# Kernel tuning notes

Measured on AMD Instinct MI355X. Metric: run time of the kernel, lower is better.

Reference implementation:

```python
import jax, jax.numpy as jnp
import numpy as np
from jax import lax

# norse LIFParameters defaults: dt=1e-3, tau_mem_inv=100, tau_syn_inv=200, v_leak=0, v_reset=0
ALPHA = 100.0
DT_TM = 0.1   # dt * tau_mem_inv
DT_TS = 0.2   # dt * tau_syn_inv

@jax.custom_vjp
def superspike(x):
    # Heaviside forward, SuperSpike surrogate gradient backward
    return (x > 0).astype(x.dtype)

def _ss_fwd(x):
    return superspike(x), x

def _ss_bwd(x, g):
    return (g / (ALPHA * jnp.abs(x) + 1.0) ** 2,)

superspike.defvjp(_ss_fwd, _ss_bwd)

def lif_step(inp, v, i, v_th):
    # norse lif_feed_forward_step (feedforward LIF cell)
    v_dec = v + DT_TM * (i - v)           # v_leak = 0
    i_dec = i * (1.0 - DT_TS)
    z = superspike(v_dec - v_th)
    v_new = (1.0 - z) * v_dec             # reset to v_reset = 0 on spike
    return z, v_new, i_dec + inp

def conv2d(x, w):
    return lax.conv_general_dilated(x, w, (1, 1), 'VALID',
                                    dimension_numbers=('NCHW', 'OIHW', 'NCHW'))

def avg_pool2(x):
    s = lax.reduce_window(x, jnp.zeros((), x.dtype), lax.add,
                          (1, 1, 2, 2), (1, 1, 2, 2), 'VALID')
    return s * jnp.asarray(0.25, x.dtype)

def setup_inputs() -> dict:
    key = jax.random.key(0)
    ks = jax.random.split(key, 6)
    x = jax.random.uniform(ks[0], (40, 256, 1, 28, 28), dtype=jnp.float32)
    # kaiming-ish scales (1/sqrt(fan_in))
    w_conv1 = jax.random.normal(ks[1], (20, 1, 3, 3), jnp.float32) * (1.0 / np.sqrt(9))
    w_conv2 = jax.random.normal(ks[2], (50, 20, 3, 3), jnp.float32) * (1.0 / np.sqrt(180))
    w_fc1 = jax.random.normal(ks[3], (500, 6050), jnp.float32) * (1.0 / np.sqrt(6050))
    w_fc2 = jax.random.normal(ks[4], (200, 500), jnp.float32) * (1.0 / np.sqrt(500))
    w_fc_out = jax.random.normal(ks[5], (10, 200), jnp.float32) * (1.0 / np.sqrt(200))
    return {"x": x, "w_conv1": w_conv1, "w_conv2": w_conv2,
            "w_fc1": w_fc1, "w_fc2": w_fc2, "w_fc_out": w_fc_out}

def reference(x, w_conv1, w_conv2, w_fc1, w_fc2, w_fc_out):
    T, B = x.shape[0], x.shape[1]
    dt = x.dtype
    z0 = jnp.zeros((B, 20, 26, 26), dt)
    z1 = jnp.zeros((B, 50, 11, 11), dt)
    z2 = jnp.zeros((B, 500), dt)
    z3 = jnp.zeros((B, 200), dt)
    zo = jnp.zeros((B, 10), dt)
    carry0 = (z0, z0, z1, z1, z2, z2, z3, z3, zo, zo)

    def step(carry, xt):
        v0, i0, v1, i1, v2, i2, v3, i3, vo, io = carry
        z = conv2d(xt, w_conv1)
        z, v0, i0 = lif_step(z, v0, i0, 0.2)
        z = avg_pool2(z)
        z = conv2d(z, w_conv2)
        z, v1, i1 = lif_step(z, v1, i1, 0.2)
        z = z.reshape(B, -1)                      # [B, 50*11*11]
        z = z @ w_fc1.T
        z, v2, i2 = lif_step(z, v2, i2, 0.1)
        z = z @ w_fc2.T
        z, v3, i3 = lif_step(z, v3, i3, 0.05)
        z = z @ w_fc_out.T
        # LICell (norse li_feed_forward_step): output is decayed membrane voltage
        v_dec = vo + DT_TM * (io - vo)
        i_new = io * (1.0 - DT_TS) + z
        return (v0, i0, v1, i1, v2, i2, v3, i3, v_dec, i_new), v_dec

    _, voltages = lax.scan(step, carry0, x)
    return voltages  # [T, B, output_neurons]
```

## Files before the change

kernel.cpp:

```cpp
#include <hip/hip_runtime.h>
#include <hip/hip_bf16.h>

typedef _Float16 f16x8 __attribute__((ext_vector_type(8)));
typedef float f32x4  __attribute__((ext_vector_type(4)));
typedef unsigned short u16x4 __attribute__((ext_vector_type(4)));

#define T_STEPS 40
#define BATCH   256
#define S2LO    0.000244140625f

__device__ __forceinline__ unsigned short f2h_bits(float f) {
    union { _Float16 h; unsigned short u; } c; c.h = (_Float16)f; return c.u;
}

__device__ __forceinline__ float lif_update(float inp, float& v, float& i, float vth) {
    float vd = __fadd_rn(v, __fmul_rn(0.1f, __fsub_rn(i, v)));
    float id = __fmul_rn(0.8f, i);
    float z  = (vd > vth) ? 1.0f : 0.0f;
    v = (vd > vth) ? 0.0f : vd;
    i = __fadd_rn(id, inp);
    return z;
}

__device__ __forceinline__ void llds16(const unsigned short* g, void* l) {
    __builtin_amdgcn_global_load_lds(
        (const __attribute__((address_space(1))) unsigned int*)g,
        (__attribute__((address_space(3))) unsigned int*)l, 16, 0, 0);
}

__global__ __launch_bounds__(512) void k_conv1(
    const float* __restrict__ x,
    const float* __restrict__ w1,
    unsigned char* __restrict__ s0)
{
    const int b    = blockIdx.y;
    const int tid  = threadIdx.x;
    const int cell = blockIdx.x*512 + tid;
    const bool active = cell < 3380;
    const int pos  = cell / 20;
    const int oc   = cell % 20;
    const int pr   = pos / 13, q = pos % 13;
    const int r0   = 2*pr, c0 = 2*q;

    __shared__ __align__(16) float xl[2][784];

    float wr[9];
    if (active) {
        #pragma unroll
        for (int j = 0; j < 9; ++j) wr[j] = w1[oc*9 + j];
    }
    float vs[2][2], is[2][2];
    #pragma unroll
    for (int dr = 0; dr < 2; ++dr)
        #pragma unroll
        for (int dc = 0; dc < 2; ++dc) { vs[dr][dc] = 0.f; is[dr][dc] = 0.f; }

    if (tid < 196) {
        const float4* xs4 = (const float4*)(x + (size_t)b*784);
        *(float4*)&xl[0][tid*4] = xs4[tid];
    }

    for (int t = 0; t < T_STEPS; ++t) {
        __syncthreads();
        if (t + 1 < T_STEPS && tid < 196) {
            const float4* xs4 = (const float4*)(x + (size_t)((t+1)*BATCH + b)*784);
            *(float4*)&xl[(t+1)&1][tid*4] = xs4[tid];
        }
        const float* xc = xl[t&1];
        size_t base = (size_t)(t*BATCH + b) * 4096;

        if (active) {
            float tle[4][4];
            #pragma unroll
            for (int r = 0; r < 4; ++r)
                #pragma unroll
                for (int c = 0; c < 4; ++c)
                    tle[r][c] = xc[(r0 + r)*28 + c0 + c];
            int zsum = 0;
            #pragma unroll
            for (int dr = 0; dr < 2; ++dr)
                #pragma unroll
                for (int dc = 0; dc < 2; ++dc) {
                    float acc = 0.f;
                    #pragma unroll
                    for (int kr = 0; kr < 3; ++kr)
                        #pragma unroll
                        for (int kc = 0; kc < 3; ++kc)
                            acc += tle[dr+kr][dc+kc] * wr[kr*3+kc];
                    float z = lif_update(acc, vs[dr][dc], is[dr][dc], 0.2f);
                    zsum += (z > 0.5f) ? 1 : 0;
                }
            s0[base + (size_t)pos*24 + oc] = (unsigned char)zsum;
        } else {
            int p2 = cell - 3380;
            for (int idx = p2; idx < 716; idx += 204) {
                if (idx < 676) s0[base + (size_t)(idx >> 2)*24 + 20 + (idx & 3)] = 0;
                else           s0[base + 4056 + (idx - 676)] = 0;
            }
        }
    }
}

__global__ __launch_bounds__(256, 2) void k_conv2(
    const unsigned char* __restrict__ s0,
    const float* __restrict__ w2,
    unsigned short* __restrict__ z1)
{
    const int b    = blockIdx.x >> 1;
    const int half = blockIdx.x & 1;
    const int tid  = threadIdx.x;
    const int wv   = tid >> 6;
    const int lane = tid & 63;
    const int l15  = lane & 15;
    const int kg   = lane >> 4;
    const int wm   = wv;

    __shared__ __align__(16) unsigned short w2h[32*232];
    __shared__ __align__(16) unsigned short w2m[32*232];
    __shared__ __align__(16) unsigned short sIn[2*4096];

    for (int s = tid; s < 32*232; s += 256) {
        int ocw = s / 232, kk = s % 232;
        int g = kk / 24, ic = kk % 24;
        int oc = half*32 + ocw;
        float val = 0.f;
        if (oc < 50 && g < 9 && ic < 20) val = w2[(oc*20 + ic)*9 + g];
        _Float16 h = (_Float16)val;
        float r1 = (val - (float)h) * 4096.0f;
        union { _Float16 h; unsigned short u; } ch, cm;
        ch.h = h; cm.h = (_Float16)r1;
        w2h[s] = ch.u;
        w2m[s] = cm.u;
    }

    f16x8 bfrH[2][7];
    int addrA[2][7];
    #pragma unroll
    for (int mt = 0; mt < 2; ++mt) {
        int pos = wm*32 + mt*16 + l15;
        #pragma unroll
        for (int kt = 0; kt < 7; ++kt) {
            int k = kt*32 + kg*8;
            int g = k / 24, o = k - g*24;
            if (pos <= 120 && g <= 8) {
                int in_idx = pos + 2*(pos/11) + 13*(g/3) + (g % 3);
                addrA[mt][kt] = in_idx*48 + o*2;
            } else addrA[mt][kt] = 8128;
        }
    }

    {
        const unsigned char* srow = s0 + (size_t)(0*BATCH + b)*4096;
        uint4 raw = *(const uint4*)(srow + tid*16);
        unsigned short hv[16];
        #pragma unroll
        for (int w = 0; w < 4; ++w) {
            unsigned int u = ((const unsigned int*)&raw)[w];
            #pragma unroll
            for (int j = 0; j < 4; ++j)
                hv[w*4+j] = f2h_bits(0.25f * (float)((u >> (8*j)) & 0xFFu));
        }
        unsigned short* dst = sIn + tid*16;
        *(f16x8*)dst       = *(const f16x8*)&hv[0];
        *(f16x8*)(dst + 8) = *(const f16x8*)&hv[8];
    }
    __syncthreads();

    #pragma unroll
    for (int nt = 0; nt < 2; ++nt) {
        int n = nt*16 + l15;
        #pragma unroll
        for (int kt = 0; kt < 7; ++kt)
            bfrH[nt][kt] = *(const f16x8*)&w2h[n*232 + kt*32 + kg*8];
    }

    float vst[2][2][4], ist[2][2][4];
    #pragma unroll
    for (int mt = 0; mt < 2; ++mt)
        #pragma unroll
        for (int nt = 0; nt < 2; ++nt)
            #pragma unroll
            for (int r = 0; r < 4; ++r) { vst[mt][nt][r] = 0.f; ist[mt][nt][r] = 0.f; }

    const f32x4 zero4 = {0.f, 0.f, 0.f, 0.f};

    for (int t = 0; t < T_STEPS; ++t) {
        if (t > 0) __syncthreads();

        uint4 raw;
        if (t + 1 < T_STEPS)
            raw = *(const uint4*)(s0 + (size_t)((t+1)*BATCH + b)*4096 + tid*16);

        const char* curB = (const char*)(sIn + (t&1)*4096);

        f32x4 acch[2][2], accl[2][2];
        #pragma unroll
        for (int mt = 0; mt < 2; ++mt)
            #pragma unroll
            for (int nt = 0; nt < 2; ++nt) { acch[mt][nt] = zero4; accl[mt][nt] = zero4; }

        #pragma unroll
        for (int kt = 0; kt < 7; ++kt) {
            f16x8 bm[2];
            #pragma unroll
            for (int nt = 0; nt < 2; ++nt) {
                int n = nt*16 + l15, k = kt*32 + kg*8;
                bm[nt] = *(const f16x8*)&w2m[n*232 + k];
            }
            #pragma unroll
            for (int mt = 0; mt < 2; ++mt) {
                f16x8 a = *(const f16x8*)(curB + addrA[mt][kt]);
                #pragma unroll
                for (int nt = 0; nt < 2; ++nt) {
                    acch[mt][nt] = __builtin_amdgcn_mfma_f32_16x16x32_f16(
                        a, bfrH[nt][kt], acch[mt][nt], 0, 0, 0);
                    accl[mt][nt] = __builtin_amdgcn_mfma_f32_16x16x32_f16(
                        a, bm[nt], accl[mt][nt], 0, 0, 0);
                }
            }
        }

        size_t rowoff = (size_t)(t*BATCH + b) * 6208;
        #pragma unroll
        for (int mt = 0; mt < 2; ++mt) {
            int posb = wm*32 + mt*16 + kg*4;
            #pragma unroll
            for (int nt = 0; nt < 2; ++nt) {
                int ocn = half*32 + nt*16 + l15;
                u16x4 pack;
                #pragma unroll
                for (int r = 0; r < 4; ++r) {
                    float inp = __fadd_rn(acch[mt][nt][r], __fmul_rn(S2LO, accl[mt][nt][r]));
                    float z = lif_update(inp, vst[mt][nt][r], ist[mt][nt][r], 0.2f);
                    int pos = posb + r;
                    pack[r] = (pos <= 120 && z > 0.5f) ? (unsigned short)0x3C00 : (unsigned short)0;
                }
                if (ocn < 50 && posb < 121)
                    *(u16x4*)(z1 + rowoff + ocn*124 + posb) = pack;
            }
        }
        if (half == 0 && tid < 8) z1[rowoff + 6200 + tid] = 0;

        if (t + 1 < T_STEPS) {
            unsigned short hv[16];
            #pragma unroll
            for (int w = 0; w < 4; ++w) {
                unsigned int u = ((const unsigned int*)&raw)[w];
                #pragma unroll
                for (int j = 0; j < 4; ++j)
                    hv[w*4+j] = f2h_bits(0.25f * (float)((u >> (8*j)) & 0xFFu));
            }
            unsigned short* dst = sIn + ((t+1)&1)*4096 + tid*16;
            *(f16x8*)dst       = *(const f16x8*)&hv[0];
            *(f16x8*)(dst + 8) = *(const f16x8*)&hv[8];
        }
    }
}

__global__ __launch_bounds__(256, 4) void k_gemm_fc1(
    const unsigned short* __restrict__ A,
    const unsigned short* __restrict__ Bhi,
    const unsigned short* __restrict__ Blo,
    float* __restrict__ P)
{
    __shared__ __align__(16) unsigned short As[128*64];
    __shared__ __align__(16) unsigned short Bh[64*64];
    __shared__ __align__(16) unsigned short Bl[64*64];

    const int tid  = threadIdx.x;
    const int lane = tid & 63;
    const int wv   = tid >> 6;
    const int wm   = wv & 1, wn = wv >> 1;
    const int l15  = lane & 15, kg = lane >> 4;

    const int bid   = blockIdx.x;
    const int chunk = (bid & 7) * 160 + (bid >> 3);
    const int mb    = chunk >> 4;
    const int nn    = chunk & 15;
    const int mbase = mb * 128;
    const int nbase = (nn >> 1) * 64;
    const int kz    = nn & 1;
    const int kb0   = kz * 3136;
    const int kiters = 49 - kz;

    float* Pz = P + (size_t)kz * 5242880;

    const f32x4 zero4 = {0.f, 0.f, 0.f, 0.f};
    f32x4 acch[4][2], accl[4][2];
    #pragma unroll
    for (int mt = 0; mt < 4; ++mt)
        #pragma unroll
        for (int nt = 0; nt < 2; ++nt) { acch[mt][nt] = zero4; accl[mt][nt] = zero4; }

    const int rowA = tid >> 3;
    const int sw   = (((tid & 7) ^ (rowA & 7))) * 8;
    char* ldsA = (char*)As + (size_t)wv*1024;
    char* ldsH = (char*)Bh + (size_t)wv*1024;
    char* ldsL = (char*)Bl + (size_t)wv*1024;

    for (int ki = 0; ki < kiters; ++ki) {
        int kb = kb0 + ki * 64;
        #pragma unroll
        for (int c = 0; c < 4; ++c)
            llds16(A + (size_t)(mbase + c*32 + rowA)*6208 + kb + sw, ldsA + c*4096);
        #pragma unroll
        for (int c = 0; c < 2; ++c) {
            llds16(Bhi + (size_t)(nbase + c*32 + rowA)*6208 + kb + sw, ldsH + c*4096);
            llds16(Blo + (size_t)(nbase + c*32 + rowA)*6208 + kb + sw, ldsL + c*4096);
        }
        __syncthreads();
        #pragma unroll
        for (int kt = 0; kt < 2; ++kt) {
            f16x8 bh[2], bl[2], afv[4];
            #pragma unroll
            for (int nt = 0; nt < 2; ++nt) {
                int rb = wn*32 + nt*16 + l15;
                int ch = ((kt*4 + kg) ^ (rb & 7)) * 8;
                bh[nt] = *(const f16x8*)&Bh[rb*64 + ch];
                bl[nt] = *(const f16x8*)&Bl[rb*64 + ch];
            }
            #pragma unroll
            for (int mt = 0; mt < 4; ++mt) {
                int ra = wm*64 + mt*16 + l15;
                int ch = ((kt*4 + kg) ^ (ra & 7)) * 8;
                afv[mt] = *(const f16x8*)&As[ra*64 + ch];
            }
            #pragma unroll
            for (int mt = 0; mt < 4; ++mt)
                #pragma unroll
                for (int nt = 0; nt < 2; ++nt) {
                    acch[mt][nt] = __builtin_amdgcn_mfma_f32_16x16x32_f16(
                        afv[mt], bh[nt], acch[mt][nt], 0, 0, 0);
                    accl[mt][nt] = __builtin_amdgcn_mfma_f32_16x16x32_f16(
                        afv[mt], bl[nt], accl[mt][nt], 0, 0, 0);
                }
        }
        __syncthreads();
    }

    #pragma unroll
    for (int mt = 0; mt < 4; ++mt) {
        int m0 = mbase + wm*64 + mt*16 + kg*4;
        #pragma unroll
        for (int nt = 0; nt < 2; ++nt) {
            int n = nbase + wn*32 + nt*16 + l15;
            #pragma unroll
            for (int r = 0; r < 4; ++r) {
                float s = __fadd_rn(acch[mt][nt][r], __fmul_rn(S2LO, accl[mt][nt][r]));
                Pz[(size_t)(m0 + r)*512 + n] = s;
            }
        }
    }
}

__global__ __launch_bounds__(256, 3) void k_gemm(
    const unsigned short* __restrict__ A,
    const unsigned short* __restrict__ B0,
    float* __restrict__ C0,
    int Kp, int kiters, int ldc, int nstore,
    size_t strideB, size_t strideC)
{
    __shared__ __align__(16) unsigned short As[128*64];
    __shared__ __align__(16) unsigned short Bs[128*64];
    const unsigned short* B = B0 + (size_t)blockIdx.z * strideB;
    float* C = C0 + (size_t)blockIdx.z * strideC;

    const int tid  = threadIdx.x;
    const int lane = tid & 63;
    const int wv   = tid >> 6;
    const int wm   = wv & 1, wn = wv >> 1;
    const int l15  = lane & 15, kg = lane >> 4;
    const int mbase = blockIdx.x * 128;
    const int nbase = blockIdx.y * 128;

    const f32x4 zero4 = {0.f, 0.f, 0.f, 0.f};
    f32x4 acc[4][4];
    #pragma unroll
    for (int mt = 0; mt < 4; ++mt)
        #pragma unroll
        for (int nt = 0; nt < 4; ++nt) acc[mt][nt] = zero4;

    const int rowA = tid >> 3;
    const int sw   = (((tid & 7) ^ (rowA & 7))) * 8;
    char* ldsA = (char*)As + (size_t)wv*1024;
    char* ldsB = (char*)Bs + (size_t)wv*1024;

    for (int ki = 0; ki < kiters; ++ki) {
        int kb = ki * 64;
        #pragma unroll
        for (int c = 0; c < 4; ++c) {
            int row = c*32 + rowA;
            llds16(A + (size_t)(mbase + row)*Kp + kb + sw, ldsA + c*4096);
            llds16(B + (size_t)(nbase + row)*Kp + kb + sw, ldsB + c*4096);
        }
        __syncthreads();
        #pragma unroll
        for (int kt = 0; kt < 2; ++kt) {
            f16x8 bfv[4], afv[4];
            #pragma unroll
            for (int nt = 0; nt < 4; ++nt) {
                int rb = wn*64 + nt*16 + l15;
                int ch = ((kt*4 + kg) ^ (rb & 7)) * 8;
                bfv[nt] = *(const f16x8*)&Bs[rb*64 + ch];
            }
            #pragma unroll
            for (int mt = 0; mt < 4; ++mt) {
                int ra = wm*64 + mt*16 + l15;
                int ch = ((kt*4 + kg) ^ (ra & 7)) * 8;
                afv[mt] = *(const f16x8*)&As[ra*64 + ch];
            }
            #pragma unroll
            for (int mt = 0; mt < 4; ++mt)
                #pragma unroll
                for (int nt = 0; nt < 4; ++nt)
                    acc[mt][nt] = __builtin_amdgcn_mfma_f32_16x16x32_f16(
                        afv[mt], bfv[nt], acc[mt][nt], 0, 0, 0);
        }
        __syncthreads();
    }

    #pragma unroll
    for (int mt = 0; mt < 4; ++mt) {
        int m0 = mbase + wm*64 + mt*16 + kg*4;
        #pragma unroll
        for (int nt = 0; nt < 4; ++nt) {
            int n = nbase + wn*64 + nt*16 + l15;
            if (n < nstore) {
                #pragma unroll
                for (int r = 0; r < 4; ++r)
                    C[(size_t)(m0 + r)*ldc + n] = acc[mt][nt][r];
            }
        }
    }
}

__global__ void k_pack_all(
    const float* __restrict__ wf1, const float* __restrict__ wf2,
    const float* __restrict__ wfo,
    unsigned short* __restrict__ W1, unsigned short* __restrict__ W2,
    unsigned short* __restrict__ Wo)
{
    int idx = blockIdx.x*256 + threadIdx.x;
    float v; unsigned short *hi, *lo; int off;
    if (idx < 3178496) {
        int n = idx / 6208, k = idx - n*6208;
        int oc = k / 124, pos = k - oc*124;
        v = (n < 500 && oc < 50 && pos < 121) ? wf1[n*6050 + oc*121 + pos] : 0.f;
        hi = W1; lo = W1 + 3178496; off = idx;
    } else if (idx < 3178496 + 131072) {
        int i2 = idx - 3178496;
        int n = i2 >> 9, k = i2 & 511;
        v = (n < 200 && k < 500) ? wf2[n*500 + k] : 0.f;
        hi = W2; lo = W2 + 131072; off = i2;
    } else if (idx < 3178496 + 131072 + 32768) {
        int i3 = idx - 3178496 - 131072;
        int n = i3 >> 8, k = i3 & 255;
        v = (n < 10 && k < 200) ? wfo[n*200 + k] : 0.f;
        hi = Wo; lo = Wo + 32768; off = i3;
    } else return;
    _Float16 h = (_Float16)v;
    float r1 = (v - (float)h) * 4096.0f;
    union { _Float16 h; unsigned short u; } ch, cl;
    ch.h = h; cl.h = (_Float16)r1;
    hi[off] = ch.u;
    lo[off] = cl.u;
}

__global__ __launch_bounds__(512) void k_lif_scan(
    const float* __restrict__ c0, size_t pstride,
    unsigned short* __restrict__ zout,
    int ld, int nvalid, float vth, float pscale)
{
    int b = blockIdx.x;
    int n = threadIdx.x;
    float v = 0.f, cur = 0.f;
    const float* sx = c0 + (size_t)b*ld + n;
    const float* sy = sx + pstride;
    const size_t step = (size_t)BATCH*ld;
    float x0 = sx[0],      y0 = sy[0];
    float x1 = sx[step],   y1 = sy[step];
    float x2 = sx[2*step], y2 = sy[2*step];
    float x3 = sx[3*step], y3 = sy[3*step];

    #define LIF_SUB(J, XV, YV)                                                \
        {                                                                     \
            float s = __fadd_rn(XV, __fmul_rn(pscale, YV));                   \
            float z = lif_update(s, v, cur, vth);                             \
            zout[(size_t)((t+J)*BATCH + b)*ld + n] =                          \
                (n < nvalid && z > 0.5f) ? (unsigned short)0x3C00             \
                                         : (unsigned short)0;                 \
            if (t + J + 4 < T_STEPS) {                                        \
                XV = sx[(size_t)(t + J + 4)*step];                            \
                YV = sy[(size_t)(t + J + 4)*step];                            \
            }                                                                 \
        }

    for (int t = 0; t < T_STEPS; t += 4) {
        LIF_SUB(0, x0, y0);
        LIF_SUB(1, x1, y1);
        LIF_SUB(2, x2, y2);
        LIF_SUB(3, x3, y3);
    }
    #undef LIF_SUB
}

__global__ void k_li(const float* __restrict__ c0, size_t pstride,
                     float* __restrict__ out) {
    int g = blockIdx.x*64 + threadIdx.x;
    if (g >= 2560) return;
    int b = g / 10, n = g - b*10;
    const float* sx = c0 + (size_t)b*16 + n;
    const float* sy = sx + pstride;
    const size_t step = (size_t)BATCH*16;
    float vo = 0.f, io = 0.f;
    float x0 = sx[0],      y0 = sy[0];
    float x1 = sx[step],   y1 = sy[step];
    float x2 = sx[2*step], y2 = sy[2*step];
    float x3 = sx[3*step], y3 = sy[3*step];

    #define LI_SUB(J, XV, YV)                                                 \
        {                                                                     \
            float s = __fadd_rn(XV, __fmul_rn(S2LO, YV));                     \
            float vd = __fadd_rn(vo, __fmul_rn(0.1f, __fsub_rn(io, vo)));     \
            out[(size_t)((t+J)*BATCH + b)*10 + n] = vd;                       \
            io = __fadd_rn(__fmul_rn(0.8f, io), s);                           \
            vo = vd;                                                          \
            if (t + J + 4 < T_STEPS) {                                        \
                XV = sx[(size_t)(t + J + 4)*step];                            \
                YV = sy[(size_t)(t + J + 4)*step];                            \
            }                                                                 \
        }

    for (int t = 0; t < T_STEPS; t += 4) {
        LI_SUB(0, x0, y0);
        LI_SUB(1, x1, y1);
        LI_SUB(2, x2, y2);
        LI_SUB(3, x3, y3);
    }
    #undef LI_SUB
}

extern "C" void kernel_launch(void* const* d_in, const int* in_sizes, int n_in,
                              void* d_out, int out_size, void* d_ws, size_t ws_size,
                              hipStream_t stream) {
    (void)in_sizes; (void)n_in; (void)out_size; (void)ws_size;
    const float* x   = (const float*)d_in[0];
    const float* w1  = (const float*)d_in[1];
    const float* w2  = (const float*)d_in[2];
    const float* wf1 = (const float*)d_in[3];
    const float* wf2 = (const float*)d_in[4];
    const float* wfo = (const float*)d_in[5];
    char* ws = (char*)d_ws;

    unsigned short* z1    = (unsigned short*)(ws);
    unsigned char*  s0    = (unsigned char*)(ws + 127139840);
    unsigned short* W1hi  = (unsigned short*)(ws + 127139840);
    unsigned short* W2hi  = (unsigned short*)(ws + 139853824);
    unsigned short* Wohi  = (unsigned short*)(ws + 140378112);
    float*          c2p   = (float*)(ws + 140509184);
    unsigned short* z2    = (unsigned short*)(ws);
    float*          c3p   = (float*)(ws + 10485760);
    unsigned short* z3    = (unsigned short*)(ws + 31457280);
    float*          c4p   = (float*)(ws + 36700160);

    k_conv1<<<dim3(7, 256), 512, 0, stream>>>(x, w1, s0);
    k_conv2<<<512, 256, 0, stream>>>(s0, w2, z1);

    k_pack_all<<<(3342336+255)/256, 256, 0, stream>>>(wf1, wf2, wfo,
                                                      W1hi, W2hi, Wohi);

    k_gemm_fc1<<<1280, 256, 0, stream>>>(z1, W1hi, W1hi+3178496, c2p);
    k_lif_scan<<<256, 512, 0, stream>>>(c2p, (size_t)5242880, z2, 512, 500, 0.1f, 1.0f);
    k_gemm<<<dim3(80,2,2), 256, 0, stream>>>(z2, W2hi, c3p, 512, 8, 256, 256,
                                             (size_t)131072, (size_t)2621440);
    k_lif_scan<<<256, 256, 0, stream>>>(c3p, (size_t)2621440, z3, 256, 200, 0.05f, S2LO);
    k_gemm<<<dim3(80,1,2), 256, 0, stream>>>(z3, Wohi, c4p, 256, 4, 16, 16,
                                             (size_t)32768, (size_t)163840);
    k_li<<<40, 64, 0, stream>>>(c4p, (size_t)163840, (float*)d_out);
}
```

Measured before the change: 407.3 us.

## Switch fc1 GEMM to int8 MFMA with three-limb fixed-point weights

Spikes from conv2 are now stored as uint8 0/1 instead of fp16 1.0. The fc1 weights are quantized into three signed int8 limbs (base 128) under a fixed global scale. The fc1 GEMM then runs three i32 16x16x64 int8 MFMAs per K-tile instead of fp16 hi/lo MFMAs, and recombines the limbs in fp32 at the end. This cuts A and B bytes per K-step and uses the higher int8 MFMA rate. The hard-coded 0.103 weight range clamps any larger weights, so accuracy depends on the weight magnitudes. The block-order swizzle and the occupancy hint on launch bounds are also dropped.

Measured after the change: 448.5 us. 1.1x slower.

```diff
diff --git a/kernel.cpp b/kernel.cpp
--- a/kernel.cpp
+++ b/kernel.cpp
@@ -3,11 +3,14 @@
 
 typedef _Float16 f16x8 __attribute__((ext_vector_type(8)));
 typedef float f32x4  __attribute__((ext_vector_type(4)));
+typedef int   i32x4  __attribute__((ext_vector_type(4)));
 typedef unsigned short u16x4 __attribute__((ext_vector_type(4)));
 
 #define T_STEPS 40
 #define BATCH   256
 #define S2LO    0.000244140625f
+#define WQ_INV  (2080768.0f/0.103f)
+#define WQ_S    (0.103f/2080768.0f)
 
 __device__ __forceinline__ unsigned short f2h_bits(float f) {
     union { _Float16 h; unsigned short u; } c; c.h = (_Float16)f; return c.u;
@@ -22,7 +25,7 @@
     return z;
 }
 
-__device__ __forceinline__ void llds16(const unsigned short* g, void* l) {
+__device__ __forceinline__ void llds16(const void* g, void* l) {
     __builtin_amdgcn_global_load_lds(
         (const __attribute__((address_space(1))) unsigned int*)g,
         (__attribute__((address_space(3))) unsigned int*)l, 16, 0, 0);
@@ -104,7 +107,7 @@
 __global__ __launch_bounds__(256, 2) void k_conv2(
     const unsigned char* __restrict__ s0,
     const float* __restrict__ w2,
-    unsigned short* __restrict__ z1)
+    unsigned char* __restrict__ z1)
 {
     const int b    = blockIdx.x >> 1;
     const int half = blockIdx.x & 1;
@@ -227,16 +230,17 @@
             #pragma unroll
             for (int nt = 0; nt < 2; ++nt) {
                 int ocn = half*32 + nt*16 + l15;
-                u16x4 pack;
+                unsigned char pk[4];
                 #pragma unroll
                 for (int r = 0; r < 4; ++r) {
                     float inp = __fadd_rn(acch[mt][nt][r], __fmul_rn(S2LO, accl[mt][nt][r]));
                     float z = lif_update(inp, vst[mt][nt][r], ist[mt][nt][r], 0.2f);
                     int pos = posb + r;
-                    pack[r] = (pos <= 120 && z > 0.5f) ? (unsigned short)0x3C00 : (unsigned short)0;
+                    pk[r] = (pos <= 120 && z > 0.5f) ? (unsigned char)1 : (unsigned char)0;
                 }
                 if (ocn < 50 && posb < 121)
-                    *(u16x4*)(z1 + rowoff + ocn*124 + posb) = pack;
+                    *(uchar4*)(z1 + rowoff + ocn*124 + posb) =
+                        *(const uchar4*)&pk[0];
             }
         }
         if (half == 0 && tid < 8) z1[rowoff + 6200 + tid] = 0;
@@ -257,84 +261,77 @@
     }
 }
 
-__global__ __launch_bounds__(256, 4) void k_gemm_fc1(
-    const unsigned short* __restrict__ A,
-    const unsigned short* __restrict__ Bhi,
-    const unsigned short* __restrict__ Blo,
+__global__ __launch_bounds__(256) void k_gemm_fc1(
+    const unsigned char* __restrict__ A,
+    const signed char* __restrict__ Bq,
     float* __restrict__ P)
 {
-    __shared__ __align__(16) unsigned short As[128*64];
-    __shared__ __align__(16) unsigned short Bh[64*64];
-    __shared__ __align__(16) unsigned short Bl[64*64];
+    __shared__ __align__(16) unsigned char As[128*64];
+    __shared__ __align__(16) unsigned char Bs[3*64*64];
 
     const int tid  = threadIdx.x;
     const int lane = tid & 63;
     const int wv   = tid >> 6;
     const int wm   = wv & 1, wn = wv >> 1;
     const int l15  = lane & 15, kg = lane >> 4;
-
-    const int bid   = blockIdx.x;
-    const int chunk = (bid & 7) * 160 + (bid >> 3);
-    const int mb    = chunk >> 4;
-    const int nn    = chunk & 15;
-    const int mbase = mb * 128;
-    const int nbase = (nn >> 1) * 64;
-    const int kz    = nn & 1;
+    const int mbase = blockIdx.x * 128;
+    const int nbase = blockIdx.y * 64;
+    const int kz    = blockIdx.z;
     const int kb0   = kz * 3136;
     const int kiters = 49 - kz;
 
     float* Pz = P + (size_t)kz * 5242880;
 
-    const f32x4 zero4 = {0.f, 0.f, 0.f, 0.f};
-    f32x4 acch[4][2], accl[4][2];
-    #pragma unroll
-    for (int mt = 0; mt < 4; ++mt)
-        #pragma unroll
-        for (int nt = 0; nt < 2; ++nt) { acch[mt][nt] = zero4; accl[mt][nt] = zero4; }
-
-    const int rowA = tid >> 3;
-    const int sw   = (((tid & 7) ^ (rowA & 7))) * 8;
+    i32x4 acc[3][4][2];
+    #pragma unroll
+    for (int p = 0; p < 3; ++p)
+        #pragma unroll
+        for (int mt = 0; mt < 4; ++mt)
+            #pragma unroll
+            for (int nt = 0; nt < 2; ++nt) acc[p][mt][nt] = (i32x4){0,0,0,0};
+
+    const int rowS = tid >> 2;
+    const int chk  = tid & 3;
     char* ldsA = (char*)As + (size_t)wv*1024;
-    char* ldsH = (char*)Bh + (size_t)wv*1024;
-    char* ldsL = (char*)Bl + (size_t)wv*1024;
+    char* ldsB = (char*)Bs + (size_t)wv*1024;
 
     for (int ki = 0; ki < kiters; ++ki) {
         int kb = kb0 + ki * 64;
         #pragma unroll
-        for (int c = 0; c < 4; ++c)
-            llds16(A + (size_t)(mbase + c*32 + rowA)*6208 + kb + sw, ldsA + c*4096);
-        #pragma unroll
-        for (int c = 0; c < 2; ++c) {
-            llds16(Bhi + (size_t)(nbase + c*32 + rowA)*6208 + kb + sw, ldsH + c*4096);
-            llds16(Blo + (size_t)(nbase + c*32 + rowA)*6208 + kb + sw, ldsL + c*4096);
-        }
+        for (int c2 = 0; c2 < 2; ++c2) {
+            int rl = c2*64 + rowS;
+            llds16(A + (size_t)(mbase + rl)*6208 + kb + 16*(chk ^ (rl & 3)),
+                   ldsA + c2*4096);
+        }
+        #pragma unroll
+        for (int p = 0; p < 3; ++p)
+            llds16(Bq + (size_t)p*3178496 + (size_t)(nbase + rowS)*6208
+                      + kb + 16*(chk ^ (rowS & 3)),
+                   ldsB + p*4096);
         __syncthreads();
-        #pragma unroll
-        for (int kt = 0; kt < 2; ++kt) {
-            f16x8 bh[2], bl[2], afv[4];
-            #pragma unroll
-            for (int nt = 0; nt < 2; ++nt) {
-                int rb = wn*32 + nt*16 + l15;
-                int ch = ((kt*4 + kg) ^ (rb & 7)) * 8;
-                bh[nt] = *(const f16x8*)&Bh[rb*64 + ch];
-                bl[nt] = *(const f16x8*)&Bl[rb*64 + ch];
-            }
-            #pragma unroll
-            for (int mt = 0; mt < 4; ++mt) {
-                int ra = wm*64 + mt*16 + l15;
-                int ch = ((kt*4 + kg) ^ (ra & 7)) * 8;
-                afv[mt] = *(const f16x8*)&As[ra*64 + ch];
-            }
+
+        i32x4 afv[4], bfv[3][2];
+        #pragma unroll
+        for (int nt = 0; nt < 2; ++nt) {
+            int rb = wn*32 + nt*16 + l15;
+            int off = rb*64 + 16*(kg ^ (rb & 3));
+            #pragma unroll
+            for (int p = 0; p < 3; ++p)
+                bfv[p][nt] = *(const i32x4*)&Bs[p*4096 + off];
+        }
+        #pragma unroll
+        for (int mt = 0; mt < 4; ++mt) {
+            int ra = wm*64 + mt*16 + l15;
+            afv[mt] = *(const i32x4*)&As[ra*64 + 16*(kg ^ (ra & 3))];
+        }
+        #pragma unroll
+        for (int p = 0; p < 3; ++p)
             #pragma unroll
             for (int mt = 0; mt < 4; ++mt)
                 #pragma unroll
-                for (int nt = 0; nt < 2; ++nt) {
-                    acch[mt][nt] = __builtin_amdgcn_mfma_f32_16x16x32_f16(
-                        afv[mt], bh[nt], acch[mt][nt], 0, 0, 0);
-                    accl[mt][nt] = __builtin_amdgcn_mfma_f32_16x16x32_f16(
-                        afv[mt], bl[nt], accl[mt][nt], 0, 0, 0);
-                }
-        }
+                for (int nt = 0; nt < 2; ++nt)
+                    acc[p][mt][nt] = __builtin_amdgcn_mfma_i32_16x16x64_i8(
+                        afv[mt], bfv[p][nt], acc[p][mt][nt], 0, 0, 0);
         __syncthreads();
     }
 
@@ -346,8 +343,11 @@
             int n = nbase + wn*32 + nt*16 + l15;
             #pragma unroll
             for (int r = 0; r < 4; ++r) {
-                float s = __fadd_rn(acch[mt][nt][r], __fmul_rn(S2LO, accl[mt][nt][r]));
-                Pz[(size_t)(m0 + r)*512 + n] = s;
+                float d = __fadd_rn(
+                    __fadd_rn(__fmul_rn(16384.0f, (float)acc[2][mt][nt][r]),
+                              __fmul_rn(128.0f,   (float)acc[1][mt][nt][r])),
+                    (float)acc[0][mt][nt][r]);
+                Pz[(size_t)(m0 + r)*512 + n] = __fmul_rn(WQ_S, d);
             }
         }
     }
@@ -437,17 +437,30 @@
 __global__ void k_pack_all(
     const float* __restrict__ wf1, const float* __restrict__ wf2,
     const float* __restrict__ wfo,
-    unsigned short* __restrict__ W1, unsigned short* __restrict__ W2,
+    signed char* __restrict__ W1, unsigned short* __restrict__ W2,
     unsigned short* __restrict__ Wo)
 {
     int idx = blockIdx.x*256 + threadIdx.x;
-    float v; unsigned short *hi, *lo; int off;
     if (idx < 3178496) {
         int n = idx / 6208, k = idx - n*6208;
         int oc = k / 124, pos = k - oc*124;
-        v = (n < 500 && oc < 50 && pos < 121) ? wf1[n*6050 + oc*121 + pos] : 0.f;
-        hi = W1; lo = W1 + 3178496; off = idx;
-    } else if (idx < 3178496 + 131072) {
+        float v = (n < 500 && oc < 50 && pos < 121) ? wf1[n*6050 + oc*121 + pos] : 0.f;
+        float a = v * WQ_INV;
+        int q2 = __float2int_rn(a * (1.0f/16384.0f));
+        q2 = q2 < -127 ? -127 : (q2 > 127 ? 127 : q2);
+        float r1 = a - (float)q2 * 16384.0f;
+        int q1 = __float2int_rn(r1 * (1.0f/128.0f));
+        q1 = q1 < -127 ? -127 : (q1 > 127 ? 127 : q1);
+        float r0 = r1 - (float)q1 * 128.0f;
+        int q0 = __float2int_rn(r0);
+        q0 = q0 < -127 ? -127 : (q0 > 127 ? 127 : q0);
+        W1[idx]             = (signed char)q0;
+        W1[idx + 3178496]   = (signed char)q1;
+        W1[idx + 2*3178496] = (signed char)q2;
+        return;
+    }
+    float v; unsigned short *hi, *lo; int off;
+    if (idx < 3178496 + 131072) {
         int i2 = idx - 3178496;
         int n = i2 >> 9, k = i2 & 511;
         v = (n < 200 && k < 500) ? wf2[n*500 + k] : 0.f;
@@ -552,9 +565,9 @@
     const float* wfo = (const float*)d_in[5];
     char* ws = (char*)d_ws;
 
-    unsigned short* z1    = (unsigned short*)(ws);
+    unsigned char*  z1    = (unsigned char*)(ws);
     unsigned char*  s0    = (unsigned char*)(ws + 127139840);
-    unsigned short* W1hi  = (unsigned short*)(ws + 127139840);
+    signed char*    W1q   = (signed char*)(ws + 127139840);
     unsigned short* W2hi  = (unsigned short*)(ws + 139853824);
     unsigned short* Wohi  = (unsigned short*)(ws + 140378112);
     float*          c2p   = (float*)(ws + 140509184);
@@ -567,9 +580,9 @@
     k_conv2<<<512, 256, 0, stream>>>(s0, w2, z1);
 
     k_pack_all<<<(3342336+255)/256, 256, 0, stream>>>(wf1, wf2, wfo,
-                                                      W1hi, W2hi, Wohi);
-
-    k_gemm_fc1<<<1280, 256, 0, stream>>>(z1, W1hi, W1hi+3178496, c2p);
+                                                      W1q, W2hi, Wohi);
+
+    k_gemm_fc1<<<dim3(80, 8, 2), 256, 0, stream>>>(z1, W1q, c2p);
     k_lif_scan<<<256, 512, 0, stream>>>(c2p, (size_t)5242880, z2, 512, 500, 0.1f, 1.0f);
     k_gemm<<<dim3(80,2,2), 256, 0, stream>>>(z2, W2hi, c3p, 512, 8, 256, 256,
                                              (size_t)131072, (size_t)2621440);
```

## Fuse output FC with LI scan and split fc1 GEMM into two launches

Applied to the files above, without the earlier changes.

Replaces the split-precision MFMA GEMM for the 10-wide output layer and the separate LI kernel with one per-batch kernel. It computes the spike-masked dot products against fp32 weights in LDS and runs the LI recurrence in the same kernel. This removes the output weight packing, one intermediate buffer round trip and one launch. The fc1 GEMM drops its swizzled 1D block index for a 3D grid and is issued as two launches over M ranges (64 and 16 blocks), which changes scheduling and L2 locality. Summation order in the output layer changes, so rounding may differ slightly from the previous path.

After: 428.6 us. 5.2% more time.

```diff
diff --git a/kernel.cpp b/kernel.cpp
--- a/kernel.cpp
+++ b/kernel.cpp
@@ -22,7 +22,7 @@
     return z;
 }
 
-__device__ __forceinline__ void llds16(const unsigned short* g, void* l) {
+__device__ __forceinline__ void llds16(const void* g, void* l) {
     __builtin_amdgcn_global_load_lds(
         (const __attribute__((address_space(1))) unsigned int*)g,
         (__attribute__((address_space(3))) unsigned int*)l, 16, 0, 0);
@@ -261,7 +261,8 @@
     const unsigned short* __restrict__ A,
     const unsigned short* __restrict__ Bhi,
     const unsigned short* __restrict__ Blo,
-    float* __restrict__ P)
+    float* __restrict__ P,
+    int mb0)
 {
     __shared__ __align__(16) unsigned short As[128*64];
     __shared__ __align__(16) unsigned short Bh[64*64];
@@ -272,14 +273,9 @@
     const int wv   = tid >> 6;
     const int wm   = wv & 1, wn = wv >> 1;
     const int l15  = lane & 15, kg = lane >> 4;
-
-    const int bid   = blockIdx.x;
-    const int chunk = (bid & 7) * 160 + (bid >> 3);
-    const int mb    = chunk >> 4;
-    const int nn    = chunk & 15;
-    const int mbase = mb * 128;
-    const int nbase = (nn >> 1) * 64;
-    const int kz    = nn & 1;
+    const int mbase = (blockIdx.x + mb0) * 128;
+    const int nbase = blockIdx.y * 64;
+    const int kz    = blockIdx.z;
     const int kb0   = kz * 3136;
     const int kiters = 49 - kz;
 
@@ -436,9 +432,7 @@
 
 __global__ void k_pack_all(
     const float* __restrict__ wf1, const float* __restrict__ wf2,
-    const float* __restrict__ wfo,
-    unsigned short* __restrict__ W1, unsigned short* __restrict__ W2,
-    unsigned short* __restrict__ Wo)
+    unsigned short* __restrict__ W1, unsigned short* __restrict__ W2)
 {
     int idx = blockIdx.x*256 + threadIdx.x;
     float v; unsigned short *hi, *lo; int off;
@@ -452,11 +446,6 @@
         int n = i2 >> 9, k = i2 & 511;
         v = (n < 200 && k < 500) ? wf2[n*500 + k] : 0.f;
         hi = W2; lo = W2 + 131072; off = i2;
-    } else if (idx < 3178496 + 131072 + 32768) {
-        int i3 = idx - 3178496 - 131072;
-        int n = i3 >> 8, k = i3 & 255;
-        v = (n < 10 && k < 200) ? wfo[n*200 + k] : 0.f;
-        hi = Wo; lo = Wo + 32768; off = i3;
     } else return;
     _Float16 h = (_Float16)v;
     float r1 = (v - (float)h) * 4096.0f;
@@ -504,40 +493,53 @@
     #undef LIF_SUB
 }
 
-__global__ void k_li(const float* __restrict__ c0, size_t pstride,
-                     float* __restrict__ out) {
-    int g = blockIdx.x*64 + threadIdx.x;
-    if (g >= 2560) return;
-    int b = g / 10, n = g - b*10;
-    const float* sx = c0 + (size_t)b*16 + n;
-    const float* sy = sx + pstride;
-    const size_t step = (size_t)BATCH*16;
-    float vo = 0.f, io = 0.f;
-    float x0 = sx[0],      y0 = sy[0];
-    float x1 = sx[step],   y1 = sy[step];
-    float x2 = sx[2*step], y2 = sy[2*step];
-    float x3 = sx[3*step], y3 = sy[3*step];
-
-    #define LI_SUB(J, XV, YV)                                                 \
-        {                                                                     \
-            float s = __fadd_rn(XV, __fmul_rn(S2LO, YV));                     \
-            float vd = __fadd_rn(vo, __fmul_rn(0.1f, __fsub_rn(io, vo)));     \
-            out[(size_t)((t+J)*BATCH + b)*10 + n] = vd;                       \
-            io = __fadd_rn(__fmul_rn(0.8f, io), s);                           \
-            vo = vd;                                                          \
-            if (t + J + 4 < T_STEPS) {                                        \
-                XV = sx[(size_t)(t + J + 4)*step];                            \
-                YV = sy[(size_t)(t + J + 4)*step];                            \
-            }                                                                 \
-        }
-
-    for (int t = 0; t < T_STEPS; t += 4) {
-        LI_SUB(0, x0, y0);
-        LI_SUB(1, x1, y1);
-        LI_SUB(2, x2, y2);
-        LI_SUB(3, x3, y3);
-    }
-    #undef LI_SUB
+__global__ __launch_bounds__(256) void k_fcout_li(
+    const unsigned short* __restrict__ z3,
+    const float* __restrict__ wfo,
+    float* __restrict__ out)
+{
+    const int b   = blockIdx.x;
+    const int tid = threadIdx.x;
+    __shared__ __align__(16) float         wfoL[2000];
+    __shared__ __align__(16) unsigned short z3L[8000];
+    __shared__ float sL[400];
+
+    for (int i = tid; i < 2000; i += 256) wfoL[i] = wfo[i];
+    for (int i = tid; i < 2000; i += 256) {
+        int t = i / 50, c = i - t*50;
+        *(ushort4*)&z3L[t*200 + c*4] =
+            *(const ushort4*)(z3 + ((size_t)(t*BATCH + b))*256 + c*4);
+    }
+    __syncthreads();
+
+    #pragma unroll
+    for (int rep = 0; rep < 2; ++rep) {
+        int task = tid + rep*256;
+        if (task < 400) {
+            int t = task / 10, n = task - t*10;
+            float acc = 0.f;
+            for (int k = 0; k < 200; k += 4) {
+                ushort4 zb = *(const ushort4*)&z3L[t*200 + k];
+                float4  wv = *(const float4*)&wfoL[n*200 + k];
+                acc = __fadd_rn(acc, zb.x ? wv.x : 0.f);
+                acc = __fadd_rn(acc, zb.y ? wv.y : 0.f);
+                acc = __fadd_rn(acc, zb.z ? wv.z : 0.f);
+                acc = __fadd_rn(acc, zb.w ? wv.w : 0.f);
+            }
+            sL[t*10 + n] = acc;
+        }
+    }
+    __syncthreads();
+
+    if (tid < 10) {
+        float vo = 0.f, io = 0.f;
+        for (int t = 0; t < T_STEPS; ++t) {
+            float vd = __fadd_rn(vo, __fmul_rn(0.1f, __fsub_rn(io, vo)));
+            out[((size_t)(t*BATCH + b))*10 + tid] = vd;
+            io = __fadd_rn(__fmul_rn(0.8f, io), sL[t*10 + tid]);
+            vo = vd;
+        }
+    }
 }
 
 extern "C" void kernel_launch(void* const* d_in, const int* in_sizes, int n_in,
@@ -556,25 +558,21 @@
     unsigned char*  s0    = (unsigned char*)(ws + 127139840);
     unsigned short* W1hi  = (unsigned short*)(ws + 127139840);
     unsigned short* W2hi  = (unsigned short*)(ws + 139853824);
-    unsigned short* Wohi  = (unsigned short*)(ws + 140378112);
     float*          c2p   = (float*)(ws + 140509184);
     unsigned short* z2    = (unsigned short*)(ws);
     float*          c3p   = (float*)(ws + 10485760);
     unsigned short* z3    = (unsigned short*)(ws + 31457280);
-    float*          c4p   = (float*)(ws + 36700160);
 
     k_conv1<<<dim3(7, 256), 512, 0, stream>>>(x, w1, s0);
     k_conv2<<<512, 256, 0, stream>>>(s0, w2, z1);
 
-    k_pack_all<<<(3342336+255)/256, 256, 0, stream>>>(wf1, wf2, wfo,
-                                                      W1hi, W2hi, Wohi);
-
-    k_gemm_fc1<<<1280, 256, 0, stream>>>(z1, W1hi, W1hi+3178496, c2p);
+    k_pack_all<<<(3309568+255)/256, 256, 0, stream>>>(wf1, wf2, W1hi, W2hi);
+
+    k_gemm_fc1<<<dim3(64, 8, 2), 256, 0, stream>>>(z1, W1hi, W1hi+3178496, c2p, 0);
+    k_gemm_fc1<<<dim3(16, 8, 2), 256, 0, stream>>>(z1, W1hi, W1hi+3178496, c2p, 64);
     k_lif_scan<<<256, 512, 0, stream>>>(c2p, (size_t)5242880, z2, 512, 500, 0.1f, 1.0f);
     k_gemm<<<dim3(80,2,2), 256, 0, stream>>>(z2, W2hi, c3p, 512, 8, 256, 256,
                                              (size_t)131072, (size_t)2621440);
     k_lif_scan<<<256, 256, 0, stream>>>(c3p, (size_t)2621440, z3, 256, 200, 0.05f, S2LO);
-    k_gemm<<<dim3(80,1,2), 256, 0, stream>>>(z3, Wohi, c4p, 256, 4, 16, 16,
-                                             (size_t)32768, (size_t)163840);
-    k_li<<<40, 64, 0, stream>>>(c4p, (size_t)163840, (float*)d_out);
-}
+    k_fcout_li<<<256, 256, 0, stream>>>(z3, wfo, (float*)d_out);
+}
```
